# Performance work log

Hardware: AMD Instinct MI355X
Metric: run time of the kernel (lower is better)

The kernel has to match this reference:

```python
import jax, jax.numpy as jnp
import numpy as np

B, S, IN = 8, 512, 128
D, H, DK, DV, DFF, L = 512, 8, 64, 64, 2048, 4
LOCAL = 64
EPS = 1e-5


def setup_inputs() -> dict:
    key = jax.random.key(0)
    ks = jax.random.split(key, 12)
    w = lambda k, shape: (jax.random.normal(k, shape, jnp.float32) * 0.02)
    return dict(
        x=jax.random.normal(ks[0], (B, S, IN), jnp.float32),
        We=w(ks[1], (IN, D)), be=jnp.zeros((D,), jnp.float32),
        Wq=w(ks[2], (L, D, H * DK)), bq=jnp.zeros((L, H * DK), jnp.float32),
        Wk=w(ks[3], (L, D, H * DK)), bk=jnp.zeros((L, H * DK), jnp.float32),
        Wv=w(ks[4], (L, D, H * DV)), bv=jnp.zeros((L, H * DV), jnp.float32),
        Wo=w(ks[5], (L, H * DV, D)), bo=jnp.zeros((L, D), jnp.float32),
        ln1_g=jnp.ones((L, D), jnp.float32), ln1_b=jnp.zeros((L, D), jnp.float32),
        W1=w(ks[6], (L, D, DFF)), b1=jnp.zeros((L, DFF), jnp.float32),
        W2=w(ks[7], (L, DFF, D)), b2=jnp.zeros((L, D), jnp.float32),
        ln2_g=jnp.ones((L, D), jnp.float32), ln2_b=jnp.zeros((L, D), jnp.float32),
    )


def _layernorm(x, g, b):
    m = jnp.mean(x, -1, keepdims=True)
    v = jnp.mean((x - m) ** 2, -1, keepdims=True)
    return (x - m) / jnp.sqrt(v + EPS) * g + b


def _gelu(x):
    # GELU tanh approximation exactly as in the torch module
    return 0.5 * x * (1.0 + jnp.tanh(np.sqrt(2.0 / np.pi) * (x + 0.044715 * x ** 3)))


def _sincos_pe():
    pos = jnp.arange(S, dtype=jnp.float32)[:, None]
    div = jnp.exp(jnp.arange(0, D, 2, dtype=jnp.float32) * (-np.log(10000.0) / D))
    pe = jnp.zeros((S, D), jnp.float32)
    pe = pe.at[:, 0::2].set(jnp.sin(pos * div))
    pe = pe.at[:, 1::2].set(jnp.cos(pos * div))
    return pe


def _forward(x, We, be, Wq, bq, Wk, bk, Wv, bv, Wo, bo,
             ln1_g, ln1_b, W1, b1, W2, b2, ln2_g, ln2_b):
    h = x @ We + be + _sincos_pe()  # [B,S,D]
    idx = jnp.arange(S)
    # local band mask: positions farther than LOCAL are masked with -1e9
    mask = jnp.abs(idx[:, None] - idx[None, :]) > LOCAL  # [S,S] bool

    def mha(hin, l):
        q = (hin @ Wq[l] + bq[l]).reshape(B, S, H, DK).transpose(0, 2, 1, 3)
        k = (hin @ Wk[l] + bk[l]).reshape(B, S, H, DK).transpose(0, 2, 1, 3)
        v = (hin @ Wv[l] + bv[l]).reshape(B, S, H, DV).transpose(0, 2, 1, 3)
        scores = jnp.einsum('bhqd,bhkd->bhqk', q, k) / np.sqrt(DK)
        scores = jnp.where(mask, -1e9, scores)
        a = jax.nn.softmax(scores, axis=-1)
        ctx = jnp.einsum('bhqk,bhkd->bhqd', a, v)
        ctx = ctx.transpose(0, 2, 1, 3).reshape(B, S, H * DV)
        out = ctx @ Wo[l] + bo[l]
        return _layernorm(out + hin, ln1_g[l], ln1_b[l]), a

    attns = []
    for l in range(L):
        h, a = mha(h, l)
        h, a = mha(h, l)  # local=True: second pass with the SAME weights
        ff = _gelu(h @ W1[l] + b1[l]) @ W2[l] + b2[l]
        h = _layernorm(ff + h, ln2_g[l], ln2_b[l])
        attns.append(a)
    attns = jnp.stack(attns).transpose(1, 0, 2, 3, 4)  # [B,L,H,S,S]
    return h, attns


def reference(x, We, be, Wq, bq, Wk, bk, Wv, bv, Wo, bo,
              ln1_g, ln1_b, W1, b1, W2, b2, ln2_g, ln2_b):
    return _forward(x, We, be, Wq, bq, Wk, bk, Wv, bv, Wo, bo,
                    ln1_g, ln1_b, W1, b1, W2, b2, ln2_g, ln2_b)
```

## Files before the change

### kernel.cpp

```cpp
#include <hip/hip_runtime.h>

using bf16 = __bf16;
using bf16x8 = __attribute__((ext_vector_type(8))) __bf16;
using bf16x4 = __attribute__((ext_vector_type(4))) __bf16;
using f32x4  = __attribute__((ext_vector_type(4))) float;

#define AS1(p) ((const __attribute__((address_space(1))) unsigned int*)(p))
#define AS3(p) ((__attribute__((address_space(3))) unsigned int*)(p))

template<int N> __device__ __forceinline__ void wait_vmcnt() {
    if constexpr (N == 0) asm volatile("s_waitcnt vmcnt(0)" ::: "memory");
    else if constexpr (N == 3) asm volatile("s_waitcnt vmcnt(3)" ::: "memory");
    else if constexpr (N == 4) asm volatile("s_waitcnt vmcnt(4)" ::: "memory");
    else if constexpr (N == 6) asm volatile("s_waitcnt vmcnt(6)" ::: "memory");
}

template<int TM, int EPI>
__global__ __launch_bounds__(256, 3)
void gemm_kernel(const bf16* __restrict__ A, const bf16* __restrict__ WT,
                 const float* __restrict__ bias, bf16* __restrict__ Cbf,
                 float* __restrict__ Cf, const float* __restrict__ PE,
                 int K, int ldc, int gx, int q8)
{
    constexpr int NA  = TM / 16;
    constexpr int NCH = NA + 8;
    constexpr int CPW = NCH / 4;
    constexpr int MI  = TM / 32;
    constexpr int ASZ = TM * 32;
    constexpr int BSZ = 128 * 32;
    __shared__ bf16 Asm[2 * ASZ];
    __shared__ bf16 Bsm[2 * BSZ];
    const int tid = threadIdx.x;
    const int lane = tid & 63;
    const int w  = tid >> 6;
    const int wr = w >> 1, wc = w & 1;
    const int l4 = lane & 15, lg = lane >> 4;

    const int bid = blockIdx.x;
    const int s  = (bid & 7) * q8 + (bid >> 3);
    const int by = s / gx, bx = s - by * gx;
    const size_t m0 = (size_t)by * TM;
    const size_t n0 = (size_t)bx * 128;

    f32x4 acc[MI][4] = {};

    const bf16* src[CPW];
    bf16* dst0[CPW];
    int step[CPW];
    #pragma unroll
    for (int ci = 0; ci < CPW; ++ci) {
        const int c = w * CPW + ci;
        if (c < NA) {
            src[ci]  = A + (m0 + (size_t)(c * 16 + (lane >> 2))) * K + (lane & 3) * 8;
            dst0[ci] = Asm + c * 512;
            step[ci] = ASZ;
        } else {
            src[ci]  = WT + (n0 + (size_t)((c - NA) * 16 + (lane >> 2))) * K + (lane & 3) * 8;
            dst0[ci] = Bsm + (c - NA) * 512;
            step[ci] = BSZ;
        }
    }
    const bf16* Ar = &Asm[(wr * (TM / 2) + l4) * 32 + lg * 8];
    const bf16* Br = &Bsm[(wc * 64 + l4) * 32 + lg * 8];

    #pragma unroll
    for (int ci = 0; ci < CPW; ++ci) {
        __builtin_amdgcn_global_load_lds(AS1(src[ci]), AS3(dst0[ci]), 16, 0, 0);
        src[ci] += 32;
    }

    const int nt = K >> 5;
    int cur = 0;
    for (int t = 0; t < nt; ++t) {
        if (t + 1 < nt) {
            #pragma unroll
            for (int ci = 0; ci < CPW; ++ci) {
                __builtin_amdgcn_global_load_lds(AS1(src[ci]),
                                                 AS3(dst0[ci] + (cur ^ 1) * step[ci]), 16, 0, 0);
                src[ci] += 32;
            }
            wait_vmcnt<CPW>();
        } else {
            wait_vmcnt<0>();
        }
        __builtin_amdgcn_s_barrier();
        const bf16* Ac = Ar + cur * ASZ;
        const bf16* Bc = Br + cur * BSZ;
        bf16x8 aF[MI], bF[4];
        #pragma unroll
        for (int i = 0; i < MI; ++i) aF[i] = *(const bf16x8*)(Ac + i * 512);
        #pragma unroll
        for (int i = 0; i < 4; ++i) bF[i] = *(const bf16x8*)(Bc + i * 512);
        #pragma unroll
        for (int mi = 0; mi < MI; ++mi)
            #pragma unroll
            for (int ni = 0; ni < 4; ++ni)
                acc[mi][ni] = __builtin_amdgcn_mfma_f32_16x16x32_bf16(
                    aF[mi], bF[ni], acc[mi][ni], 0, 0, 0);
        asm volatile("s_waitcnt lgkmcnt(0)" ::: "memory");
        __builtin_amdgcn_s_barrier();
        cur ^= 1;
    }

    #pragma unroll
    for (int ni = 0; ni < 4; ++ni) {
        const int col = (int)n0 + wc * 64 + ni * 16 + l4;
        const float bv = bias[col];
        #pragma unroll
        for (int mi = 0; mi < MI; ++mi) {
            const int row0 = (int)m0 + wr * (TM / 2) + mi * 16 + lg * 4;
            #pragma unroll
            for (int r = 0; r < 4; ++r) {
                float v = acc[mi][ni][r] + bv;
                const int row = row0 + r;
                if (EPI == 1) {
                    float u = 1.5957691216057308f * (v + 0.044715f * v * v * v);
                    v = v / (1.0f + __expf(-u));
                }
                if (EPI == 2) {
                    v += PE[((row & 511) << 9) + col];
                    Cf[(size_t)row * ldc + col] = v;
                }
                Cbf[(size_t)row * ldc + col] = (bf16)v;
            }
        }
    }
}

template<int WRITE_ATTN>
__global__ __launch_bounds__(256, 2)
void attn_kernel(const bf16* __restrict__ qkv, bf16* __restrict__ ctx,
                 float* __restrict__ attn_out )
{
    __shared__ bf16 Ks[192 * 72];
    __shared__ bf16 Vt[64 * 200];
    __shared__ bf16 Ps[64 * 200];
    const int tid = threadIdx.x;
    const int lane = tid & 63, w = tid >> 6;
    const int l4 = lane & 15, lg = lane >> 4;
    const int bh = blockIdx.y, ib = blockIdx.x;
    const int b = bh >> 3, hd = bh & 7;
    const int i0 = ib * 64;
    const int j0 = (i0 >= 64) ? i0 - 64 : 0;
    const int j1 = (i0 + 128 <= 512) ? i0 + 128 : 512;
    const int W = j1 - j0;
    const size_t rowb = (size_t)b * 512;

    if (WRITE_ATTN) {
        float* arow = attn_out + (size_t)b * 8388608 + (size_t)hd * 262144 +
                      (size_t)i0 * 512;
        const int zr = tid >> 2, p = tid & 3;
        f32x4 z = {0.f, 0.f, 0.f, 0.f};
        f32x4* rp = (f32x4*)(arow + (size_t)zr * 512);
        for (int c = p; c < (j0 >> 2); c += 4) rp[c] = z;
        for (int c = (j1 >> 2) + p; c < 128; c += 4) rp[c] = z;
    }

    for (int it = 0; it < 6; ++it) {
        int chunk = tid + it * 256;
        int j = chunk >> 3, k0 = (chunk & 7) * 8;
        if (j < W) {
            bf16x8 v = *(const bf16x8*)(qkv + (rowb + j0 + j) * 1536 + 512 + hd * 64 + k0);
            *(bf16x8*)(&Ks[j * 72 + k0]) = v;
        }
    }
    for (int it = 0; it < 6; ++it) {
        int chunk = tid + it * 256;
        int j = chunk >> 3, d0 = (chunk & 7) * 8;
        if (j < W) {
            bf16x8 v = *(const bf16x8*)(qkv + (rowb + j0 + j) * 1536 + 1024 + hd * 64 + d0);
            #pragma unroll
            for (int e = 0; e < 8; ++e) Vt[(d0 + e) * 200 + j] = v[e];
        }
    }
    bf16x8 qF0, qF1;
    {
        const bf16* qrow = qkv + (rowb + i0 + w * 16 + l4) * 1536 + hd * 64;
        qF0 = *(const bf16x8*)(qrow + lg * 8);
        qF1 = *(const bf16x8*)(qrow + 32 + lg * 8);
    }
    __syncthreads();

    f32x4 s[12];
    #pragma unroll
    for (int t = 0; t < 12; ++t) s[t] = (f32x4){0.f, 0.f, 0.f, 0.f};
    const int NT = W >> 4;
    for (int t = 0; t < NT; ++t) {
        const bf16* kb = &Ks[(t * 16 + l4) * 72];
        bf16x8 b0 = *(const bf16x8*)(kb + lg * 8);
        bf16x8 b1 = *(const bf16x8*)(kb + 32 + lg * 8);
        s[t] = __builtin_amdgcn_mfma_f32_16x16x32_bf16(qF0, b0, s[t], 0, 0, 0);
        s[t] = __builtin_amdgcn_mfma_f32_16x16x32_bf16(qF1, b1, s[t], 0, 0, 0);
    }
    const int irow0 = i0 + w * 16 + lg * 4;
    float pm[4] = {-3e38f, -3e38f, -3e38f, -3e38f};
    for (int t = 0; t < NT; ++t) {
        int jg = j0 + t * 16 + l4;
        #pragma unroll
        for (int r = 0; r < 4; ++r) {
            int dd = irow0 + r - jg;
            float sv = s[t][r] * 0.125f;
            if (dd > 64 || dd < -64) sv = -1e30f;
            s[t][r] = sv;
            pm[r] = fmaxf(pm[r], sv);
        }
    }
    #pragma unroll
    for (int d = 1; d < 16; d <<= 1)
        #pragma unroll
        for (int r = 0; r < 4; ++r) pm[r] = fmaxf(pm[r], __shfl_xor(pm[r], d));
    float ps[4] = {0.f, 0.f, 0.f, 0.f};
    for (int t = 0; t < NT; ++t)
        #pragma unroll
        for (int r = 0; r < 4; ++r) {
            float p = __expf(s[t][r] - pm[r]);
            s[t][r] = p;
            ps[r] += p;
        }
    #pragma unroll
    for (int d = 1; d < 16; d <<= 1)
        #pragma unroll
        for (int r = 0; r < 4; ++r) ps[r] += __shfl_xor(ps[r], d);
    float rinv[4];
    #pragma unroll
    for (int r = 0; r < 4; ++r) rinv[r] = 1.0f / ps[r];

    for (int t = 0; t < NT; ++t) {
        #pragma unroll
        for (int r = 0; r < 4; ++r) {
            float p = s[t][r] * rinv[r];
            Ps[(w * 16 + lg * 4 + r) * 200 + t * 16 + l4] = (bf16)p;
            if (WRITE_ATTN) {
                size_t off = (size_t)b * 8388608 + (size_t)hd * 262144 +
                             (size_t)(i0 + w * 16 + lg * 4 + r) * 512 +
                             (size_t)(j0 + t * 16 + l4);
                attn_out[off] = p;
            }
        }
    }
    f32x4 o[4] = {};
    const int KS = W >> 5;
    for (int ks = 0; ks < KS; ++ks) {
        bf16x8 aF = *(const bf16x8*)(&Ps[(w * 16 + l4) * 200 + ks * 32 + lg * 8]);
        #pragma unroll
        for (int ni = 0; ni < 4; ++ni) {
            bf16x8 bF = *(const bf16x8*)(&Vt[(ni * 16 + l4) * 200 + ks * 32 + lg * 8]);
            o[ni] = __builtin_amdgcn_mfma_f32_16x16x32_bf16(aF, bF, o[ni], 0, 0, 0);
        }
    }
    #pragma unroll
    for (int ni = 0; ni < 4; ++ni)
        #pragma unroll
        for (int r = 0; r < 4; ++r)
            ctx[(rowb + i0 + w * 16 + lg * 4 + r) * 512 + hd * 64 + ni * 16 + l4] =
                (bf16)o[ni][r];
}

__global__ __launch_bounds__(256)
void ln_kernel(const bf16* __restrict__ y, const float* hin,
               const float* __restrict__ g, const float* __restrict__ bb,
               float* hf, bf16* __restrict__ hbf)
{
    const int row = blockIdx.x * 4 + (threadIdx.x >> 6);
    const int lane = threadIdx.x & 63;
    const size_t base = (size_t)row * 512 + lane * 8;
    bf16x8 yv = *(const bf16x8*)(y + base);
    f32x4 h0 = *(const f32x4*)(hin + base);
    f32x4 h1 = *(const f32x4*)(hin + base + 4);
    float x[8];
    #pragma unroll
    for (int i = 0; i < 8; ++i) x[i] = (float)yv[i] + (i < 4 ? h0[i] : h1[i - 4]);
    float s = 0.f, q = 0.f;
    #pragma unroll
    for (int i = 0; i < 8; ++i) { s += x[i]; q += x[i] * x[i]; }
    #pragma unroll
    for (int d = 1; d < 64; d <<= 1) { s += __shfl_xor(s, d); q += __shfl_xor(q, d); }
    const float m = s * 0.001953125f;
    const float var = q * 0.001953125f - m * m;
    const float rstd = rsqrtf(var + 1e-5f);
    const int c0 = lane * 8;
    f32x4 g0 = *(const f32x4*)(g + c0), g1v = *(const f32x4*)(g + c0 + 4);
    f32x4 b0 = *(const f32x4*)(bb + c0), b1v = *(const f32x4*)(bb + c0 + 4);
    f32x4 o0, o1;
    bf16x8 ob;
    #pragma unroll
    for (int i = 0; i < 8; ++i) {
        float gg = i < 4 ? g0[i] : g1v[i - 4];
        float bv = i < 4 ? b0[i] : b1v[i - 4];
        float o = (x[i] - m) * rstd * gg + bv;
        if (i < 4) o0[i] = o; else o1[i - 4] = o;
        ob[i] = (bf16)o;
    }
    *(f32x4*)(hf + base) = o0;
    *(f32x4*)(hf + base + 4) = o1;
    *(bf16x8*)(hbf + base) = ob;
}

struct TMat { const float* src; size_t dst; int K; int N; int tile0; };
struct TDesc { TMat m[26]; };

__global__ __launch_bounds__(256)
void wtrans_kernel(TDesc d, bf16* __restrict__ wbuf)
{
    __shared__ float tile[32][33];
    int t = blockIdx.x;
    int mi = 0;
    while (t >= d.m[mi + 1].tile0) ++mi;
    const TMat mm = d.m[mi];
    const int lt = t - mm.tile0;
    const int tpr = mm.N >> 5;
    const int kt = lt / tpr, nt = lt % tpr;
    const int r = threadIdx.x >> 5, c = threadIdx.x & 31;
    #pragma unroll
    for (int it = 0; it < 4; ++it)
        tile[r + it * 8][c] =
            mm.src[(size_t)(kt * 32 + r + it * 8) * mm.N + nt * 32 + c];
    __syncthreads();
    #pragma unroll
    for (int it = 0; it < 4; ++it)
        wbuf[mm.dst + (size_t)(nt * 32 + r + it * 8) * mm.K + kt * 32 + c] =
            (bf16)tile[c][r + it * 8];
}

__global__ void bcat_kernel(const float* bq, const float* bk, const float* bv,
                            float* dst)
{
    int i = blockIdx.x * 256 + threadIdx.x;
    if (i < 6144) {
        int l = i / 1536, c = i - l * 1536;
        float v;
        if (c < 512) v = bq[l * 512 + c];
        else if (c < 1024) v = bk[l * 512 + c - 512];
        else v = bv[l * 512 + c - 1024];
        dst[i] = v;
    }
}

__global__ void f2bf_kernel(const float* __restrict__ src, bf16* __restrict__ dst,
                            int n4)
{
    int i = blockIdx.x * 256 + threadIdx.x;
    if (i < n4) {
        f32x4 v = *(const f32x4*)(src + (size_t)i * 4);
        bf16x4 o;
        #pragma unroll
        for (int e = 0; e < 4; ++e) o[e] = (bf16)v[e];
        *(bf16x4*)(dst + (size_t)i * 4) = o;
    }
}

__global__ void pe_kernel(float* __restrict__ pe)
{
    int i = blockIdx.x * 256 + threadIdx.x;
    int s = i >> 8, d2 = i & 255;
    float ang = (float)s * expf((float)(2 * d2) * -0.017988946039016f);
    pe[(s << 9) + 2 * d2]     = sinf(ang);
    pe[(s << 9) + 2 * d2 + 1] = cosf(ang);
}

extern "C" void kernel_launch(void* const* d_in, const int* in_sizes, int n_in,
                              void* d_out, int out_size, void* d_ws, size_t ws_size,
                              hipStream_t stream)
{
    const float* x   = (const float*)d_in[0];
    const float* We  = (const float*)d_in[1];
    const float* be  = (const float*)d_in[2];
    const float* Wq  = (const float*)d_in[3];
    const float* bq  = (const float*)d_in[4];
    const float* Wk  = (const float*)d_in[5];
    const float* bk  = (const float*)d_in[6];
    const float* Wv  = (const float*)d_in[7];
    const float* bv  = (const float*)d_in[8];
    const float* Wo  = (const float*)d_in[9];
    const float* bo  = (const float*)d_in[10];
    const float* g1  = (const float*)d_in[11];
    const float* b1n = (const float*)d_in[12];
    const float* W1  = (const float*)d_in[13];
    const float* b1f = (const float*)d_in[14];
    const float* W2  = (const float*)d_in[15];
    const float* b2f = (const float*)d_in[16];
    const float* g2  = (const float*)d_in[17];
    const float* b2n = (const float*)d_in[18];

    char* ws = (char*)d_ws;
    bf16* wbuf = (bf16*)ws;
    size_t off = 12648448ull * 2;
    float* bqkv = (float*)(ws + off); off += 6144ull * 4;
    float* pe   = (float*)(ws + off); off += 262144ull * 4;
    bf16* xbf   = (bf16*)(ws + off);  off += 524288ull * 2;
    float* h    = (float*)(ws + off); off += 2097152ull * 4;
    bf16* hbf   = (bf16*)(ws + off);  off += 2097152ull * 2;
    bf16* qkvb  = (bf16*)(ws + off);  off += 6291456ull * 2;
    bf16* ctx   = (bf16*)(ws + off);  off += 2097152ull * 2;
    bf16* tmp   = (bf16*)(ws + off);  off += 2097152ull * 2;
    bf16* ffn   = (bf16*)(ws + off);  off += 8388608ull * 2;
    (void)ws_size; (void)in_sizes; (void)n_in; (void)out_size;

    float* out_h = (float*)d_out;
    float* out_attn = out_h + 2097152;

    TDesc td{};
    int tile = 0, e = 0;
    auto add = [&](const float* src, size_t dst, int K, int N) {
        td.m[e].src = src; td.m[e].dst = dst; td.m[e].K = K; td.m[e].N = N;
        td.m[e].tile0 = tile; tile += (K >> 5) * (N >> 5); ++e;
    };
    add(We, 0, 128, 512);
    for (int l = 0; l < 4; ++l) {
        size_t base = 65536 + (size_t)l * 3145728;
        add(Wq + (size_t)l * 262144,  base + 0,       512, 512);
        add(Wk + (size_t)l * 262144,  base + 262144,  512, 512);
        add(Wv + (size_t)l * 262144,  base + 524288,  512, 512);
        add(Wo + (size_t)l * 262144,  base + 786432,  512, 512);
        add(W1 + (size_t)l * 1048576, base + 1048576, 512, 2048);
        add(W2 + (size_t)l * 1048576, base + 2097152, 2048, 512);
    }
    td.m[e].tile0 = tile;

    wtrans_kernel<<<dim3(tile), dim3(256), 0, stream>>>(td, wbuf);
    bcat_kernel<<<dim3(24), dim3(256), 0, stream>>>(bq, bk, bv, bqkv);
    f2bf_kernel<<<dim3(512), dim3(256), 0, stream>>>(x, xbf, 131072);
    pe_kernel<<<dim3(512), dim3(256), 0, stream>>>(pe);

    gemm_kernel<64, 2><<<dim3(256), dim3(256), 0, stream>>>(
        xbf, wbuf, be, hbf, h, pe, 128, 512, 4, 32);

    for (int l = 0; l < 4; ++l) {
        const bf16* WqkvT = wbuf + 65536 + (size_t)l * 3145728;
        const bf16* WoT   = WqkvT + 786432;
        const bf16* W1T   = WqkvT + 1048576;
        const bf16* W2T   = WqkvT + 2097152;
        for (int pass = 0; pass < 2; ++pass) {
            gemm_kernel<128, 0><<<dim3(384), dim3(256), 0, stream>>>(
                hbf, WqkvT, bqkv + l * 1536, qkvb, (float*)nullptr, (float*)nullptr,
                512, 1536, 12, 48);
            if (pass == 0)
                attn_kernel<0><<<dim3(8, 64), dim3(256), 0, stream>>>(
                    qkvb, ctx, (float*)nullptr);
            else
                attn_kernel<1><<<dim3(8, 64), dim3(256), 0, stream>>>(
                    qkvb, ctx, out_attn + (size_t)l * 2097152);
            gemm_kernel<64, 0><<<dim3(256), dim3(256), 0, stream>>>(
                ctx, WoT, bo + l * 512, tmp, (float*)nullptr, (float*)nullptr,
                512, 512, 4, 32);
            ln_kernel<<<dim3(1024), dim3(256), 0, stream>>>(
                tmp, h, g1 + l * 512, b1n + l * 512, h, hbf);
        }
        gemm_kernel<128, 1><<<dim3(512), dim3(256), 0, stream>>>(
            hbf, W1T, b1f + l * 2048, ffn, (float*)nullptr, (float*)nullptr,
            512, 2048, 16, 64);
        gemm_kernel<64, 0><<<dim3(256), dim3(256), 0, stream>>>(
            ffn, W2T, b2f + l * 512, tmp, (float*)nullptr, (float*)nullptr,
            2048, 512, 4, 32);
        float* hout = (l == 3) ? out_h : h;
        ln_kernel<<<dim3(1024), dim3(256), 0, stream>>>(
            tmp, h, g2 + l * 512, b2n + l * 512, hout, hbf);
    }
}
```

Baseline: 752.2 us.

## Triple-buffer GEMM LDS pipeline and fuse prep kernels into one launch

The GEMM main loop moves from double to triple buffering in LDS. Two k-tiles are prefetched ahead via global_load_lds, and the vmcnt waits are adjusted to match, so more load latency is hidden behind MFMA work. Launch bounds for the TM=64 variant are raised to four blocks per SM. The separate bias-concat, float-to-bf16 and positional-encoding kernels are merged into one prep kernel to save launch overhead. The extra LDS per block may reduce occupancy for the TM=128 variant.

```diff
diff --git a/kernel.cpp b/kernel.cpp
--- a/kernel.cpp
+++ b/kernel.cpp
@@ -13,10 +13,11 @@
     else if constexpr (N == 3) asm volatile("s_waitcnt vmcnt(3)" ::: "memory");
     else if constexpr (N == 4) asm volatile("s_waitcnt vmcnt(4)" ::: "memory");
     else if constexpr (N == 6) asm volatile("s_waitcnt vmcnt(6)" ::: "memory");
+    else if constexpr (N == 8) asm volatile("s_waitcnt vmcnt(8)" ::: "memory");
 }
 
 template<int TM, int EPI>
-__global__ __launch_bounds__(256, 3)
+__global__ __launch_bounds__(256, TM == 64 ? 4 : 3)
 void gemm_kernel(const bf16* __restrict__ A, const bf16* __restrict__ WT,
                  const float* __restrict__ bias, bf16* __restrict__ Cbf,
                  float* __restrict__ Cf, const float* __restrict__ PE,
@@ -28,8 +29,8 @@
     constexpr int MI  = TM / 32;
     constexpr int ASZ = TM * 32;
     constexpr int BSZ = 128 * 32;
-    __shared__ bf16 Asm[2 * ASZ];
-    __shared__ bf16 Bsm[2 * BSZ];
+    __shared__ bf16 Asm[3 * ASZ];
+    __shared__ bf16 Bsm[3 * BSZ];
     const int tid = threadIdx.x;
     const int lane = tid & 63;
     const int w  = tid >> 6;
@@ -63,22 +64,26 @@
     const bf16* Ar = &Asm[(wr * (TM / 2) + l4) * 32 + lg * 8];
     const bf16* Br = &Bsm[(wc * 64 + l4) * 32 + lg * 8];
 
-    #pragma unroll
-    for (int ci = 0; ci < CPW; ++ci) {
-        __builtin_amdgcn_global_load_lds(AS1(src[ci]), AS3(dst0[ci]), 16, 0, 0);
-        src[ci] += 32;
-    }
+    auto STAGE = [&](int b) {
+        #pragma unroll
+        for (int ci = 0; ci < CPW; ++ci) {
+            __builtin_amdgcn_global_load_lds(AS1(src[ci]),
+                                             AS3(dst0[ci] + b * step[ci]), 16, 0, 0);
+            src[ci] += 32;
+        }
+    };
 
     const int nt = K >> 5;
+    STAGE(0);
+    if (nt > 1) STAGE(1);
+
     int cur = 0;
     for (int t = 0; t < nt; ++t) {
-        if (t + 1 < nt) {
-            #pragma unroll
-            for (int ci = 0; ci < CPW; ++ci) {
-                __builtin_amdgcn_global_load_lds(AS1(src[ci]),
-                                                 AS3(dst0[ci] + (cur ^ 1) * step[ci]), 16, 0, 0);
-                src[ci] += 32;
-            }
+        if (t + 2 < nt) {
+            int pb = cur - 1; if (pb < 0) pb = 2;
+            STAGE(pb);
+            wait_vmcnt<2 * CPW>();
+        } else if (t + 1 < nt) {
             wait_vmcnt<CPW>();
         } else {
             wait_vmcnt<0>();
@@ -99,7 +104,7 @@
                     aF[mi], bF[ni], acc[mi][ni], 0, 0, 0);
         asm volatile("s_waitcnt lgkmcnt(0)" ::: "memory");
         __builtin_amdgcn_s_barrier();
-        cur ^= 1;
+        cur = (cur == 2) ? 0 : cur + 1;
     }
 
     #pragma unroll
@@ -322,40 +327,36 @@
             (bf16)tile[c][r + it * 8];
 }
 
-__global__ void bcat_kernel(const float* bq, const float* bk, const float* bv,
-                            float* dst)
-{
-    int i = blockIdx.x * 256 + threadIdx.x;
-    if (i < 6144) {
-        int l = i / 1536, c = i - l * 1536;
-        float v;
-        if (c < 512) v = bq[l * 512 + c];
-        else if (c < 1024) v = bk[l * 512 + c - 512];
-        else v = bv[l * 512 + c - 1024];
-        dst[i] = v;
-    }
-}
-
-__global__ void f2bf_kernel(const float* __restrict__ src, bf16* __restrict__ dst,
-                            int n4)
-{
-    int i = blockIdx.x * 256 + threadIdx.x;
-    if (i < n4) {
-        f32x4 v = *(const f32x4*)(src + (size_t)i * 4);
+__global__ void prep_kernel(const float* __restrict__ x, bf16* __restrict__ xbf,
+                            float* __restrict__ pe,
+                            const float* bq, const float* bk, const float* bv,
+                            float* __restrict__ bqkv)
+{
+    const int bid = blockIdx.x;
+    if (bid < 512) {
+        int i = bid * 256 + threadIdx.x;
+        f32x4 v = *(const f32x4*)(x + (size_t)i * 4);
         bf16x4 o;
         #pragma unroll
         for (int e = 0; e < 4; ++e) o[e] = (bf16)v[e];
-        *(bf16x4*)(dst + (size_t)i * 4) = o;
-    }
-}
-
-__global__ void pe_kernel(float* __restrict__ pe)
-{
-    int i = blockIdx.x * 256 + threadIdx.x;
-    int s = i >> 8, d2 = i & 255;
-    float ang = (float)s * expf((float)(2 * d2) * -0.017988946039016f);
-    pe[(s << 9) + 2 * d2]     = sinf(ang);
-    pe[(s << 9) + 2 * d2 + 1] = cosf(ang);
+        *(bf16x4*)(xbf + (size_t)i * 4) = o;
+    } else if (bid < 1024) {
+        int i = (bid - 512) * 256 + threadIdx.x;
+        int s = i >> 8, d2 = i & 255;
+        float ang = (float)s * expf((float)(2 * d2) * -0.017988946039016f);
+        pe[(s << 9) + 2 * d2]     = sinf(ang);
+        pe[(s << 9) + 2 * d2 + 1] = cosf(ang);
+    } else {
+        int i = (bid - 1024) * 256 + threadIdx.x;
+        if (i < 6144) {
+            int l = i / 1536, c = i - l * 1536;
+            float v;
+            if (c < 512) v = bq[l * 512 + c];
+            else if (c < 1024) v = bk[l * 512 + c - 512];
+            else v = bv[l * 512 + c - 1024];
+            bqkv[i] = v;
+        }
+    }
 }
 
 extern "C" void kernel_launch(void* const* d_in, const int* in_sizes, int n_in,
@@ -418,9 +419,7 @@
     td.m[e].tile0 = tile;
 
     wtrans_kernel<<<dim3(tile), dim3(256), 0, stream>>>(td, wbuf);
-    bcat_kernel<<<dim3(24), dim3(256), 0, stream>>>(bq, bk, bv, bqkv);
-    f2bf_kernel<<<dim3(512), dim3(256), 0, stream>>>(x, xbf, 131072);
-    pe_kernel<<<dim3(512), dim3(256), 0, stream>>>(pe);
+    prep_kernel<<<dim3(1048), dim3(256), 0, stream>>>(x, xbf, pe, bq, bk, bv, bqkv);
 
     gemm_kernel<64, 2><<<dim3(256), dim3(256), 0, stream>>>(
         xbf, wbuf, be, hbf, h, pe, 128, 512, 4, 32);
```

New measurement: 718.9 us. 4.4% less time.
